# Optimization experiments

Hardware: AMD Instinct MI355X
Metric: run time of the kernel (lower is better)

The kernel has to match this reference:

```python
import jax, jax.numpy as jnp
import numpy as np

N_NODES = 100000
N_EDGES = 3200000
IN_F = 128
OUT_F = 64
HEADS = 8
ALPHA = 0.2  # LeakyReLU negative slope


def setup_inputs() -> dict:
    key = jax.random.key(0)
    k1, k2, k3, k4 = jax.random.split(key, 4)
    x = jax.random.normal(k1, (N_NODES, IN_F), dtype=jnp.float32)
    edges = jax.random.randint(k2, (2, N_EDGES), 0, N_NODES, dtype=jnp.int64)
    # glorot-uniform-ish scaled params, stacked over heads
    lim_W = np.sqrt(6.0 / (IN_F + OUT_F))
    lim_a = np.sqrt(6.0 / (2 * OUT_F + 1))
    W = jax.random.uniform(k3, (HEADS, IN_F, OUT_F), minval=-lim_W, maxval=lim_W, dtype=jnp.float32)
    a = jax.random.uniform(k4, (HEADS, 2 * OUT_F, 1), minval=-lim_a, maxval=lim_a, dtype=jnp.float32)
    return {"x": x, "edges": edges, "W": W, "a": a}


def reference(x, edges, W, a):
    # x: [N, in_f]; edges: [2, E]; W: [H, in_f, out_f]; a: [H, 2*out_f, 1]
    N = x.shape[0]
    src, tgt = edges[0], edges[1]
    outs = []
    for h in range(W.shape[0]):  # small fixed head count; keeps peak memory per-head
        Wh = x @ W[h]                                  # [N, F]
        # Whij @ a == Wh[src] @ a[:F] + Wh[tgt] @ a[F:], computed at node level
        a_src = Wh @ a[h, :OUT_F, 0]                   # [N]
        a_tgt = Wh @ a[h, OUT_F:, 0]                   # [N]
        e = -jax.nn.leaky_relu(a_src[src] + a_tgt[tgt], negative_slope=ALPHA)  # [E]
        e_exp = jnp.exp(e - jnp.max(e))                # global max, as in the torch code
        denom = jax.ops.segment_sum(e_exp, src, num_segments=N) + 1e-10  # [N]
        att = e_exp / denom[src]                       # [E] edge softmax over source groups
        msg = att[:, None] * Wh[tgt]                   # [E, F]
        outs.append(jax.ops.segment_sum(msg, src, num_segments=N))  # [N, F]
    return jnp.concatenate(outs, axis=1)               # concat reduction -> [N, H*F]
```

## Files before the change

kernel.cpp:

```cpp
#include <hip/hip_runtime.h>
#include <hip/hip_bf16.h>

#define N_NODES 100000
#define N_EDGES 3200000
#define IN_F 128
#define OUT_F 64
#define HEADS 8
#define ALPHA 0.2f

#define BSHIFT 7
#define NBUCK 782
#define CHUNK 2048
#define NPBLK 1563
#define XADOT_BLKS 1024

typedef __bf16 bf16x8 __attribute__((ext_vector_type(8)));
typedef float f32x4 __attribute__((ext_vector_type(4)));
typedef __attribute__((ext_vector_type(8))) unsigned short ushort8;

static __device__ __forceinline__ unsigned short f2b(float f) {
    __hip_bfloat16 h = __float2bfloat16(f);
    return __builtin_bit_cast(unsigned short, h);
}

static __device__ __forceinline__ void gll16(const void* g, void* l) {
    __builtin_amdgcn_global_load_lds(
        (const __attribute__((address_space(1))) void*)g,
        (__attribute__((address_space(3))) void*)l, 16, 0, 0);
}

__global__ __launch_bounds__(256) void k_prep(const float* __restrict__ W,
                                              const float* __restrict__ a,
                                              unsigned short* __restrict__ Wt,
                                              float* __restrict__ uvT,
                                              int* __restrict__ bhist) {
    int b = blockIdx.x, t = threadIdx.x;
    if (b < 256) {
        int idx = b * 256 + t;
        int k = idx & 127;
        int c = idx >> 7;
        int h = c >> 6;
        int f = c & 63;
        Wt[idx] = f2b(W[h * IN_F * OUT_F + k * OUT_F + f]);
    } else if (b == 256) {
#pragma unroll
        for (int j = 0; j < 4; ++j) {
            int t2 = t + j * 256;
            int h = t2 >> 7, k = t2 & 127;
            const float* Wrow = W + h * IN_F * OUT_F + k * OUT_F;
            const float* ah = a + h * 2 * OUT_F;
            float su = 0.f, sv = 0.f;
            for (int f = 0; f < OUT_F; ++f) {
                float wv = Wrow[f];
                su += wv * ah[f];
                sv += wv * ah[OUT_F + f];
            }
            uvT[k * 16 + h] = su;
            uvT[k * 16 + 8 + h] = sv;
        }
    } else {
        for (int i = t; i < NBUCK; i += 256) bhist[i] = 0;
    }
}

__global__ __launch_bounds__(256) void k_xadot(const float* __restrict__ x,
                                               const float* __restrict__ uvT,
                                               const int* __restrict__ src,
                                               unsigned short* __restrict__ xb,
                                               float* __restrict__ asrc,
                                               float* __restrict__ atgt,
                                               int* __restrict__ bhist) {
    const int b = blockIdx.x, t = threadIdx.x;
    if (b >= XADOT_BLKS) {
        __shared__ int h[NBUCK];
        for (int i = t; i < NBUCK; i += 256) h[i] = 0;
        __syncthreads();
        int cb = b - XADOT_BLKS;
        int i0 = cb * CHUNK;
        int iend = i0 + CHUNK;
        if (iend > N_EDGES) iend = N_EDGES;
        for (int i = i0 + t; i < iend; i += 256)
            atomicAdd(&h[src[i] >> BSHIFT], 1);
        __syncthreads();
        for (int i = t; i < NBUCK; i += 256)
            if (h[i]) atomicAdd(&bhist[i], h[i]);
        return;
    }
    const int lane = t & 63, wid = t >> 6;
    const int o = lane & 15, q = lane >> 4;
    float up[32];
#pragma unroll
    for (int j = 0; j < 32; ++j) up[j] = uvT[(q * 32 + j) * 16 + o];

    for (int n = b * 4 + wid; n < N_NODES; n += XADOT_BLKS * 4) {
        const float* xr = x + (size_t)n * 128;
        float2 xv2 = *reinterpret_cast<const float2*>(xr + 2 * lane);
        ushort2 pv = make_ushort2(f2b(xv2.x), f2b(xv2.y));
        *reinterpret_cast<ushort2*>(xb + (size_t)n * 128 + 2 * lane) = pv;
        float r = 0.f;
        const float4* xq = reinterpret_cast<const float4*>(xr + q * 32);
#pragma unroll
        for (int j = 0; j < 8; ++j) {
            float4 xv = xq[j];
            r = fmaf(xv.x, up[4 * j], r);
            r = fmaf(xv.y, up[4 * j + 1], r);
            r = fmaf(xv.z, up[4 * j + 2], r);
            r = fmaf(xv.w, up[4 * j + 3], r);
        }
        r += __shfl_xor(r, 16);
        r += __shfl_xor(r, 32);
        if (lane < 8) asrc[n * 8 + o] = r;
        else if (lane < 16) atgt[n * 8 + (o - 8)] = r;
    }
}

__global__ __launch_bounds__(1024) void k_bscan(const int* __restrict__ bhist,
                                                int* __restrict__ bstart,
                                                int* __restrict__ bcursor,
                                                int* __restrict__ rowptr) {
    __shared__ int s[1024];
    int t = threadIdx.x;
    int v = (t < NBUCK) ? bhist[t] : 0;
    s[t] = v;
    __syncthreads();
    for (int d = 1; d < 1024; d <<= 1) {
        int add = (t >= d) ? s[t - d] : 0;
        __syncthreads();
        s[t] += add;
        __syncthreads();
    }
    if (t < NBUCK) {
        int st = s[t] - v;
        bstart[t] = st;
        bcursor[t] = st;
    }
    if (t == 0) {
        bstart[NBUCK] = N_EDGES;
        rowptr[N_NODES] = N_EDGES;
    }
}

__global__ __launch_bounds__(256) void k_bscatter(const int* __restrict__ src,
                                                  const int* __restrict__ tgt,
                                                  int* __restrict__ bcursor,
                                                  unsigned int* __restrict__ pairs) {
    __shared__ int h[NBUCK];
    __shared__ int rsv[NBUCK];
    for (int i = threadIdx.x; i < NBUCK; i += 256) h[i] = 0;
    __syncthreads();
    int i0 = blockIdx.x * CHUNK;
    int iend = i0 + CHUNK;
    if (iend > N_EDGES) iend = N_EDGES;
    for (int i = i0 + threadIdx.x; i < iend; i += 256)
        atomicAdd(&h[src[i] >> BSHIFT], 1);
    __syncthreads();
    for (int i = threadIdx.x; i < NBUCK; i += 256) {
        int c = h[i];
        rsv[i] = c ? atomicAdd(&bcursor[i], c) : 0;
        h[i] = 0;
    }
    __syncthreads();
    for (int i = i0 + threadIdx.x; i < iend; i += 256) {
        int s = src[i];
        int b = s >> BSHIFT;
        int p = rsv[b] + atomicAdd(&h[b], 1);
        pairs[p] = ((unsigned)(s & 127) << 17) | (unsigned)tgt[i];
    }
}

__global__ __launch_bounds__(512) void k_bsort(const unsigned int* __restrict__ pairs,
                                               const int* __restrict__ bstart,
                                               int* __restrict__ rowptr,
                                               int* __restrict__ stgt) {
    __shared__ int h[128];
    __shared__ int s[128];
    int b = blockIdx.x;
    int p0 = bstart[b], p1 = bstart[b + 1];
    int n0 = b << BSHIFT;
    int t = threadIdx.x;
    if (t < 128) h[t] = 0;
    __syncthreads();
    for (int i = p0 + t; i < p1; i += 512)
        atomicAdd(&h[pairs[i] >> 17], 1);
    __syncthreads();
    int v = (t < 128) ? h[t] : 0;
    if (t < 128) s[t] = v;
    __syncthreads();
    for (int d = 1; d < 128; d <<= 1) {
        int add = (t >= d && t < 128) ? s[t - d] : 0;
        __syncthreads();
        if (t < 128) s[t] += add;
        __syncthreads();
    }
    if (t < 128) {
        int pos = p0 + s[t] - v;
        int node = n0 + t;
        if (node < N_NODES) rowptr[node] = pos;
        h[t] = pos;
    }
    __syncthreads();
    for (int i = p0 + t; i < p1; i += 512) {
        unsigned int pr = pairs[i];
        int pos = atomicAdd(&h[pr >> 17], 1);
        stgt[pos] = (int)(pr & 0x1FFFF);
    }
}

__global__ __launch_bounds__(256) void k_agg10(const int* __restrict__ rowptr,
                                               const int* __restrict__ stgt,
                                               const float* __restrict__ asrc,
                                               const float* __restrict__ atgt,
                                               const unsigned short* __restrict__ xb,
                                               unsigned short* __restrict__ aggout) {
    __shared__ char lds[4 * 5120];
    const int tid = threadIdx.x;
    const int wid = tid >> 6, lane = tid & 63;
    const int node = blockIdx.x * 4 + wid;
    if (node >= N_NODES) return;
    const int seg = lane & 15;
    const int hp = lane >> 4;
    const int base = rowptr[node], end = rowptr[node + 1];
    const float2 asr = *reinterpret_cast<const float2*>(asrc + (size_t)node * 8 + hp * 2);
    char* buf = lds + wid * 5120;

    float2 accA[4] = {}, accB[4] = {};
    float den0 = 0.f, den1 = 0.f;

    const int deg = end - base;
    const int nch = (deg + 15) >> 4;

    auto eidx = [&](int c) {
        int i = base + c * 16 + seg;
        if (i >= end) i = end - 1;
        return i;
    };
    auto stage = [&](int t16) {
        int te_a = __shfl(t16, (lane & 31) >> 1);
        gll16(atgt + (size_t)te_a * 8 + (lane & 1) * 4, buf);
#pragma unroll
        for (int p = 0; p < 4; ++p) {
            int te = __shfl(t16, p * 4 + hp);
            gll16(xb + (size_t)te * 128 + seg * 8, buf + 1024 + p * 1024);
        }
    };

#define EDGE_STEP(E) { \
        uint4 xu = *reinterpret_cast<const uint4*>(Xb + (E) * 256 + seg * 16); \
        float2 w2 = *reinterpret_cast<const float2*>(buf + (E) * 32 + hp * 8); \
        _Pragma("unroll") \
        for (int i = 0; i < 4; ++i) { \
            unsigned int u = (&xu.x)[i]; \
            float2 xv; \
            xv.x = __builtin_bit_cast(float, u << 16); \
            xv.y = __builtin_bit_cast(float, u & 0xFFFF0000u); \
            asm("v_pk_fma_f32 %0, %1, %2, %0 op_sel:[0,0,0] op_sel_hi:[1,0,1]" \
                : "+v"(accA[i]) : "v"(xv), "v"(w2)); \
            asm("v_pk_fma_f32 %0, %1, %2, %0 op_sel:[0,1,0] op_sel_hi:[1,1,1]" \
                : "+v"(accB[i]) : "v"(xv), "v"(w2)); \
        } }

    if (nch > 0) {
        int t16 = stgt[eidx(0)];
        for (int c = 0; c < nch; ++c) {
            asm volatile("s_waitcnt lgkmcnt(0)" ::: "memory");
            __builtin_amdgcn_sched_barrier(0);
            stage(t16);
            if (c + 1 < nch) t16 = stgt[eidx(c + 1)];
            asm volatile("s_waitcnt vmcnt(0)" ::: "memory");
            __builtin_amdgcn_sched_barrier(0);
            int c0 = base + c * 16;
            int cnt = end - c0;
            if (cnt > 16) cnt = 16;
            {
                float2 at2 = *reinterpret_cast<const float2*>(buf + seg * 32 + hp * 8);
                float z0 = asr.x + at2.x, z1 = asr.y + at2.y;
                float e0 = (z0 > 0.f) ? -z0 : -(ALPHA * z0);
                float e1 = (z1 > 0.f) ? -z1 : -(ALPHA * z1);
                bool ok = seg < cnt;
                float w0 = ok ? __expf(e0) : 0.f;
                float w1 = ok ? __expf(e1) : 0.f;
                den0 += w0;
                den1 += w1;
                float2 wout = {w0, w1};
                *reinterpret_cast<float2*>(buf + seg * 32 + hp * 8) = wout;
            }
            asm volatile("s_waitcnt lgkmcnt(0)" ::: "memory");
            __builtin_amdgcn_sched_barrier(0);
            const char* Xb = buf + 1024;
            if (cnt == 16) {
#pragma unroll 4
                for (int e = 0; e < 16; ++e) EDGE_STEP(e)
            } else {
                for (int e = 0; e < cnt; ++e) EDGE_STEP(e)
            }
        }
    }
#undef EDGE_STEP

    for (int d = 1; d <= 8; d <<= 1) {
        den0 += __shfl_xor(den0, d);
        den1 += __shfl_xor(den1, d);
    }
    float invA = 1.f / (den0 + 1e-10f);
    float invB = 1.f / (den1 + 1e-10f);
    ushort8 oA, oB;
#pragma unroll
    for (int i = 0; i < 4; ++i) {
        oA[2 * i] = f2b(accA[i].x * invA);
        oA[2 * i + 1] = f2b(accA[i].y * invA);
        oB[2 * i] = f2b(accB[i].x * invB);
        oB[2 * i + 1] = f2b(accB[i].y * invB);
    }
    unsigned short* op = aggout + (size_t)node * 1024 + (hp * 2) * 128 + seg * 8;
    *reinterpret_cast<ushort8*>(op) = oA;
    *reinterpret_cast<ushort8*>(op + 128) = oB;
}

#define LDK2 136
__global__ __launch_bounds__(256) void k_gemm2(const unsigned short* __restrict__ agg,
                                               const unsigned short* __restrict__ Wt,
                                               float* __restrict__ out) {
    __shared__ unsigned short Al[64 * LDK2];
    __shared__ unsigned short Bl[64 * LDK2];
    const int tid = threadIdx.x;
    const int h = blockIdx.y;
    const int r0 = blockIdx.x * 64;
    for (int it = 0; it < 4; ++it) {
        int idx = tid + it * 256;
        int r = idx >> 4, k8 = (idx & 15) << 3;
        int gr = r0 + r;
        if (gr >= N_NODES) gr = N_NODES - 1;
        *reinterpret_cast<ushort8*>(&Al[r * LDK2 + k8]) =
            *reinterpret_cast<const ushort8*>(agg + (size_t)gr * 1024 + h * 128 + k8);
    }
    for (int it = 0; it < 4; ++it) {
        int idx = tid + it * 256;
        int f = idx >> 4, k8 = (idx & 15) << 3;
        *reinterpret_cast<ushort8*>(&Bl[f * LDK2 + k8]) =
            *reinterpret_cast<const ushort8*>(Wt + (size_t)(h * 64 + f) * 128 + k8);
    }
    __syncthreads();
    const int lane = tid & 63, w = tid >> 6;
    const int l15 = lane & 15, lq = lane >> 4;
    f32x4 acc[4] = {};
    for (int ks = 0; ks < 4; ++ks) {
        int koff = ks * 32 + lq * 8;
        bf16x8 af = *reinterpret_cast<const bf16x8*>(&Al[(w * 16 + l15) * LDK2 + koff]);
#pragma unroll
        for (int n = 0; n < 4; ++n) {
            bf16x8 bf_ = *reinterpret_cast<const bf16x8*>(&Bl[(n * 16 + l15) * LDK2 + koff]);
            acc[n] = __builtin_amdgcn_mfma_f32_16x16x32_bf16(af, bf_, acc[n], 0, 0, 0);
        }
    }
    for (int n = 0; n < 4; ++n) {
        int col = h * 64 + n * 16 + l15;
        int rbase = r0 + w * 16 + lq * 4;
#pragma unroll
        for (int r2 = 0; r2 < 4; ++r2) {
            int rr = rbase + r2;
            if (rr < N_NODES) out[(size_t)rr * 512 + col] = acc[n][r2];
        }
    }
}

extern "C" void kernel_launch(void* const* d_in, const int* in_sizes, int n_in,
                              void* d_out, int out_size, void* d_ws, size_t ws_size,
                              hipStream_t stream) {
    const float* x = (const float*)d_in[0];
    const int* edges = (const int*)d_in[1];
    const float* W = (const float*)d_in[2];
    const float* a = (const float*)d_in[3];
    float* out = (float*)d_out;
    const int* src = edges;
    const int* tgt = edges + N_EDGES;

    char* ws = (char*)d_ws;
    size_t off = 0;
    auto alloc = [&](size_t bytes) -> void* {
        void* p = (void*)(ws + off);
        off += (bytes + 255) & ~(size_t)255;
        return p;
    };
    unsigned short* Wt = (unsigned short*)alloc((size_t)HEADS * OUT_F * IN_F * 2);
    float* uvT = (float*)alloc((size_t)IN_F * 16 * 4);
    unsigned short* xb = (unsigned short*)alloc((size_t)N_NODES * IN_F * 2);
    float* asrc = (float*)alloc((size_t)N_NODES * 8 * 4);
    float* atgt = (float*)alloc((size_t)N_NODES * 8 * 4);
    int* bhist = (int*)alloc((size_t)NBUCK * 4);
    int* bstart = (int*)alloc((size_t)(NBUCK + 1) * 4);
    int* bcursor = (int*)alloc((size_t)NBUCK * 4);
    int* rowptr = (int*)alloc((size_t)(N_NODES + 1) * 4);
    unsigned int* pairs = (unsigned int*)alloc((size_t)N_EDGES * 4);
    int* stgt = (int*)alloc((size_t)N_EDGES * 4);
    (void)ws_size; (void)n_in; (void)in_sizes; (void)out_size;

    k_prep<<<258, 256, 0, stream>>>(W, a, Wt, uvT, bhist);
    k_xadot<<<XADOT_BLKS + NPBLK, 256, 0, stream>>>(x, uvT, src, xb, asrc, atgt, bhist);
    k_bscan<<<1, 1024, 0, stream>>>(bhist, bstart, bcursor, rowptr);
    k_bscatter<<<NPBLK, 256, 0, stream>>>(src, tgt, bcursor, pairs);
    k_bsort<<<NBUCK, 512, 0, stream>>>(pairs, bstart, rowptr, stgt);
    k_agg10<<<25000, 256, 0, stream>>>(rowptr, stgt, asrc, atgt, xb,
                                       (unsigned short*)d_out);
    k_gemm2<<<dim3(1563, 8), 256, 0, stream>>>((const unsigned short*)d_out, Wt, out);
}
```

Before: 454.0 us.

## Process 32 edges per staging round in aggregation and enlarge GEMM row tile

The aggregation kernel now stages 32 neighbour edges per round instead of 16. The target-attention vectors and eight bf16 feature rows per stage are gathered into a larger LDS buffer, and the softmax weights are computed four heads per lane. Nodes of typical degree then need about half as many stage/wait rounds, which cuts exposed gather latency; the denominator reduction is reworked to match. The second GEMM doubles its row tile to 128, so each loaded weight tile feeds twice as many MFMAs. The cost is more LDS per block (which may lower occupancy) and more registers.

```diff
diff --git a/kernel.cpp b/kernel.cpp
--- a/kernel.cpp
+++ b/kernel.cpp
@@ -206,40 +206,42 @@
     }
 }
 
-__global__ __launch_bounds__(256) void k_agg10(const int* __restrict__ rowptr,
+__global__ __launch_bounds__(256) void k_agg11(const int* __restrict__ rowptr,
                                                const int* __restrict__ stgt,
                                                const float* __restrict__ asrc,
                                                const float* __restrict__ atgt,
                                                const unsigned short* __restrict__ xb,
                                                unsigned short* __restrict__ aggout) {
-    __shared__ char lds[4 * 5120];
+    __shared__ char lds[4 * 9216];
     const int tid = threadIdx.x;
     const int wid = tid >> 6, lane = tid & 63;
     const int node = blockIdx.x * 4 + wid;
     if (node >= N_NODES) return;
     const int seg = lane & 15;
     const int hp = lane >> 4;
+    const int e32 = lane & 31;
+    const int q2 = lane >> 5;
     const int base = rowptr[node], end = rowptr[node + 1];
-    const float2 asr = *reinterpret_cast<const float2*>(asrc + (size_t)node * 8 + hp * 2);
-    char* buf = lds + wid * 5120;
+    const int deg = end - base;
+    const float4 asr4 = *reinterpret_cast<const float4*>(asrc + (size_t)node * 8 + q2 * 4);
+    char* buf = lds + wid * 9216;
 
     float2 accA[4] = {}, accB[4] = {};
-    float den0 = 0.f, den1 = 0.f;
-
-    const int deg = end - base;
-    const int nch = (deg + 15) >> 4;
+    float4 den4 = {0.f, 0.f, 0.f, 0.f};
+
+    const int nch = (deg + 31) >> 5;
 
     auto eidx = [&](int c) {
-        int i = base + c * 16 + seg;
+        int i = base + c * 32 + e32;
         if (i >= end) i = end - 1;
         return i;
     };
-    auto stage = [&](int t16) {
-        int te_a = __shfl(t16, (lane & 31) >> 1);
-        gll16(atgt + (size_t)te_a * 8 + (lane & 1) * 4, buf);
-#pragma unroll
-        for (int p = 0; p < 4; ++p) {
-            int te = __shfl(t16, p * 4 + hp);
+    auto stage = [&](int t32) {
+        int ta = __shfl(t32, lane >> 1);
+        gll16(atgt + (size_t)ta * 8 + (lane & 1) * 4, buf);
+#pragma unroll
+        for (int p = 0; p < 8; ++p) {
+            int te = __shfl(t32, p * 4 + (lane >> 4));
             gll16(xb + (size_t)te * 128 + seg * 8, buf + 1024 + p * 1024);
         }
     };
@@ -260,36 +262,40 @@
         } }
 
     if (nch > 0) {
-        int t16 = stgt[eidx(0)];
+        int t32 = stgt[eidx(0)];
         for (int c = 0; c < nch; ++c) {
             asm volatile("s_waitcnt lgkmcnt(0)" ::: "memory");
             __builtin_amdgcn_sched_barrier(0);
-            stage(t16);
-            if (c + 1 < nch) t16 = stgt[eidx(c + 1)];
+            stage(t32);
+            if (c + 1 < nch) t32 = stgt[eidx(c + 1)];
             asm volatile("s_waitcnt vmcnt(0)" ::: "memory");
             __builtin_amdgcn_sched_barrier(0);
-            int c0 = base + c * 16;
-            int cnt = end - c0;
-            if (cnt > 16) cnt = 16;
+            int cnt = deg - c * 32;
+            if (cnt > 32) cnt = 32;
             {
-                float2 at2 = *reinterpret_cast<const float2*>(buf + seg * 32 + hp * 8);
-                float z0 = asr.x + at2.x, z1 = asr.y + at2.y;
-                float e0 = (z0 > 0.f) ? -z0 : -(ALPHA * z0);
-                float e1 = (z1 > 0.f) ? -z1 : -(ALPHA * z1);
-                bool ok = seg < cnt;
-                float w0 = ok ? __expf(e0) : 0.f;
-                float w1 = ok ? __expf(e1) : 0.f;
-                den0 += w0;
-                den1 += w1;
-                float2 wout = {w0, w1};
-                *reinterpret_cast<float2*>(buf + seg * 32 + hp * 8) = wout;
+                char* wp = buf + e32 * 32 + q2 * 16;
+                float4 at4 = *reinterpret_cast<const float4*>(wp);
+                float z0 = asr4.x + at4.x, z1 = asr4.y + at4.y;
+                float z2 = asr4.z + at4.z, z3 = asr4.w + at4.w;
+                float g0 = (z0 > 0.f) ? -z0 : -(ALPHA * z0);
+                float g1 = (z1 > 0.f) ? -z1 : -(ALPHA * z1);
+                float g2 = (z2 > 0.f) ? -z2 : -(ALPHA * z2);
+                float g3 = (z3 > 0.f) ? -z3 : -(ALPHA * z3);
+                bool ok = e32 < cnt;
+                float4 w4;
+                w4.x = ok ? __expf(g0) : 0.f;
+                w4.y = ok ? __expf(g1) : 0.f;
+                w4.z = ok ? __expf(g2) : 0.f;
+                w4.w = ok ? __expf(g3) : 0.f;
+                den4.x += w4.x; den4.y += w4.y; den4.z += w4.z; den4.w += w4.w;
+                *reinterpret_cast<float4*>(wp) = w4;
             }
             asm volatile("s_waitcnt lgkmcnt(0)" ::: "memory");
             __builtin_amdgcn_sched_barrier(0);
             const char* Xb = buf + 1024;
-            if (cnt == 16) {
+            if (cnt == 32) {
 #pragma unroll 4
-                for (int e = 0; e < 16; ++e) EDGE_STEP(e)
+                for (int e = 0; e < 32; ++e) EDGE_STEP(e)
             } else {
                 for (int e = 0; e < cnt; ++e) EDGE_STEP(e)
             }
@@ -297,10 +303,19 @@
     }
 #undef EDGE_STEP
 
-    for (int d = 1; d <= 8; d <<= 1) {
-        den0 += __shfl_xor(den0, d);
-        den1 += __shfl_xor(den1, d);
-    }
+    for (int d = 1; d <= 16; d <<= 1) {
+        den4.x += __shfl_xor(den4.x, d);
+        den4.y += __shfl_xor(den4.y, d);
+        den4.z += __shfl_xor(den4.z, d);
+        den4.w += __shfl_xor(den4.w, d);
+    }
+    int srcl = (hp >> 1) << 5;
+    float sx = __shfl(den4.x, srcl);
+    float sy = __shfl(den4.y, srcl);
+    float sz = __shfl(den4.z, srcl);
+    float sw = __shfl(den4.w, srcl);
+    float den0 = (hp & 1) ? sz : sx;
+    float den1 = (hp & 1) ? sw : sy;
     float invA = 1.f / (den0 + 1e-10f);
     float invB = 1.f / (den1 + 1e-10f);
     ushort8 oA, oB;
@@ -320,12 +335,12 @@
 __global__ __launch_bounds__(256) void k_gemm2(const unsigned short* __restrict__ agg,
                                                const unsigned short* __restrict__ Wt,
                                                float* __restrict__ out) {
-    __shared__ unsigned short Al[64 * LDK2];
+    __shared__ unsigned short Al[128 * LDK2];
     __shared__ unsigned short Bl[64 * LDK2];
     const int tid = threadIdx.x;
     const int h = blockIdx.y;
-    const int r0 = blockIdx.x * 64;
-    for (int it = 0; it < 4; ++it) {
+    const int r0 = blockIdx.x * 128;
+    for (int it = 0; it < 8; ++it) {
         int idx = tid + it * 256;
         int r = idx >> 4, k8 = (idx & 15) << 3;
         int gr = r0 + r;
@@ -342,25 +357,30 @@
     __syncthreads();
     const int lane = tid & 63, w = tid >> 6;
     const int l15 = lane & 15, lq = lane >> 4;
-    f32x4 acc[4] = {};
+    f32x4 acc[2][4] = {};
     for (int ks = 0; ks < 4; ++ks) {
         int koff = ks * 32 + lq * 8;
-        bf16x8 af = *reinterpret_cast<const bf16x8*>(&Al[(w * 16 + l15) * LDK2 + koff]);
+        bf16x8 af0 = *reinterpret_cast<const bf16x8*>(&Al[(w * 32 + l15) * LDK2 + koff]);
+        bf16x8 af1 = *reinterpret_cast<const bf16x8*>(&Al[(w * 32 + 16 + l15) * LDK2 + koff]);
 #pragma unroll
         for (int n = 0; n < 4; ++n) {
             bf16x8 bf_ = *reinterpret_cast<const bf16x8*>(&Bl[(n * 16 + l15) * LDK2 + koff]);
-            acc[n] = __builtin_amdgcn_mfma_f32_16x16x32_bf16(af, bf_, acc[n], 0, 0, 0);
-        }
-    }
-    for (int n = 0; n < 4; ++n) {
-        int col = h * 64 + n * 16 + l15;
-        int rbase = r0 + w * 16 + lq * 4;
-#pragma unroll
-        for (int r2 = 0; r2 < 4; ++r2) {
-            int rr = rbase + r2;
-            if (rr < N_NODES) out[(size_t)rr * 512 + col] = acc[n][r2];
-        }
-    }
+            acc[0][n] = __builtin_amdgcn_mfma_f32_16x16x32_bf16(af0, bf_, acc[0][n], 0, 0, 0);
+            acc[1][n] = __builtin_amdgcn_mfma_f32_16x16x32_bf16(af1, bf_, acc[1][n], 0, 0, 0);
+        }
+    }
+#pragma unroll
+    for (int m = 0; m < 2; ++m)
+#pragma unroll
+        for (int n = 0; n < 4; ++n) {
+            int col = h * 64 + n * 16 + l15;
+            int rbase = r0 + w * 32 + m * 16 + lq * 4;
+#pragma unroll
+            for (int r2 = 0; r2 < 4; ++r2) {
+                int rr = rbase + r2;
+                if (rr < N_NODES) out[(size_t)rr * 512 + col] = acc[m][n][r2];
+            }
+        }
 }
 
 extern "C" void kernel_launch(void* const* d_in, const int* in_sizes, int n_in,
@@ -399,7 +419,7 @@
     k_bscan<<<1, 1024, 0, stream>>>(bhist, bstart, bcursor, rowptr);
     k_bscatter<<<NPBLK, 256, 0, stream>>>(src, tgt, bcursor, pairs);
     k_bsort<<<NBUCK, 512, 0, stream>>>(pairs, bstart, rowptr, stgt);
-    k_agg10<<<25000, 256, 0, stream>>>(rowptr, stgt, asrc, atgt, xb,
+    k_agg11<<<25000, 256, 0, stream>>>(rowptr, stgt, asrc, atgt, xb,
                                        (unsigned short*)d_out);
-    k_gemm2<<<dim3(1563, 8), 256, 0, stream>>>((const unsigned short*)d_out, Wt, out);
-}
+    k_gemm2<<<dim3(782, 8), 256, 0, stream>>>((const unsigned short*)d_out, Wt, out);
+}
```

After: 464.9 us. 2.4% more time.
